# Kernel tuning notes

Measured on AMD Instinct MI355X. Metric: run time of the kernel, lower is better.

Reference implementation:

```python
import jax, jax.numpy as jnp
import numpy as np

B_SZ, T, D_MODEL, N_STATE = 4, 4096, 1024, 256
D_FF = ((int(8 / 3 * D_MODEL) + 7) // 8) * 8  # 2736
EPS = 1e-6


def setup_inputs() -> dict:
    key = jax.random.key(0)
    ks = jax.random.split(key, 8)
    return {
        "x": jax.random.normal(ks[0], (B_SZ, T, D_MODEL), dtype=jnp.float32),
        "log_lambda": jax.random.normal(ks[1], (N_STATE,), dtype=jnp.float32) * 0.5 + 3.0,
        "B_w": jax.random.normal(ks[2], (N_STATE, D_MODEL), dtype=jnp.float32) / np.sqrt(D_MODEL),
        "C_w": jax.random.normal(ks[3], (D_MODEL, N_STATE), dtype=jnp.float32) / np.sqrt(N_STATE),
        "D_skip": jnp.zeros((D_MODEL,), dtype=jnp.float32),
        "ssm_norm_w": jnp.ones((D_MODEL,), dtype=jnp.float32),
        "ffn_norm_w": jnp.ones((D_MODEL,), dtype=jnp.float32),
        "w1": jax.random.normal(ks[4], (D_FF, D_MODEL), dtype=jnp.float32) / np.sqrt(D_MODEL),
        "w2": jax.random.normal(ks[5], (D_MODEL, D_FF), dtype=jnp.float32) / np.sqrt(D_FF),
        "w3": jax.random.normal(ks[6], (D_FF, D_MODEL), dtype=jnp.float32) / np.sqrt(D_MODEL),
    }


def _rmsnorm(x, w):
    rms = jnp.sqrt(jnp.mean(x * x, axis=-1, keepdims=True) + EPS)
    return x / rms * w


def reference(x, log_lambda, B_w, C_w, D_skip, ssm_norm_w, ffn_norm_w, w1, w2, w3):
    # --- SSM branch ---
    u = _rmsnorm(x, ssm_norm_w)                       # [B,T,D]
    lam = jax.nn.sigmoid(log_lambda)                  # [N]
    Bu = jnp.einsum("btd,nd->btn", u, B_w)            # [B,T,N]

    def step(h, bu_t):                                 # h: [B,N], bu_t: [B,N]
        h = lam * h + bu_t
        return h, h

    h0 = jnp.zeros((x.shape[0], log_lambda.shape[0]), dtype=x.dtype)
    _, hs = jax.lax.scan(step, h0, jnp.swapaxes(Bu, 0, 1))  # hs: [T,B,N]
    hs = jnp.swapaxes(hs, 0, 1)                        # [B,T,N]
    y = jnp.einsum("btn,dn->btd", hs, C_w) + D_skip * u
    x = x + y

    # --- FFN branch (SwiGLU) ---
    z = _rmsnorm(x, ffn_norm_w)
    gate = jax.nn.silu(jnp.einsum("btd,fd->btf", z, w1))
    val = jnp.einsum("btd,fd->btf", z, w3)
    ffn = jnp.einsum("btf,df->btd", gate * val, w2)
    return x + ffn
```

## Files before the change

### kernel.cpp

```cpp
#include <hip/hip_runtime.h>
#include <hip/hip_bf16.h>
#include <cstdint>

#define BSZ   4
#define TLEN  4096
#define DM    1024
#define NS    256
#define DFF   2736
#define DFFP  2816
#define NPK   5632
#define NCHUNK 64
#define CLEN   64

typedef __attribute__((ext_vector_type(8))) short bf16x8;
typedef __attribute__((ext_vector_type(4))) float f32x4;

__device__ __forceinline__ float bf2f(ushort u) {
  union { unsigned int i; float f; } v; v.i = ((unsigned int)u) << 16; return v.f;
}
__device__ __forceinline__ ushort f2bf(float f) {
  union { float f; unsigned int i; } v; v.f = f;
  unsigned int r = v.i + 0x7FFFu + ((v.i >> 16) & 1u);
  return (ushort)(r >> 16);
}
__device__ __forceinline__ void gload16(const ushort* g, ushort* l) {
  __builtin_amdgcn_global_load_lds((const __attribute__((address_space(1))) void*)g,
                                   (__attribute__((address_space(3))) void*)l, 16, 0, 0);
}

__global__ void convert_pad(const float* __restrict__ src, ushort* __restrict__ dst,
                            int srcR, int srcC, int dstR, int dstC) {
  long total = (long)dstR * dstC / 4;
  for (long q = (long)blockIdx.x * blockDim.x + threadIdx.x; q < total;
       q += (long)gridDim.x * blockDim.x) {
    long e = q * 4;
    int r = (int)(e / dstC);
    int c = (int)(e % dstC);
    ushort4 o;
    float v0 = (r < srcR && c + 0 < srcC) ? src[(long)r * srcC + c + 0] : 0.f;
    float v1 = (r < srcR && c + 1 < srcC) ? src[(long)r * srcC + c + 1] : 0.f;
    float v2 = (r < srcR && c + 2 < srcC) ? src[(long)r * srcC + c + 2] : 0.f;
    float v3 = (r < srcR && c + 3 < srcC) ? src[(long)r * srcC + c + 3] : 0.f;
    o.x = f2bf(v0); o.y = f2bf(v1); o.z = f2bf(v2); o.w = f2bf(v3);
    *(ushort4*)(dst + e) = o;
  }
}

__global__ void pack_w13(const float* __restrict__ w1, const float* __restrict__ w3,
                         ushort* __restrict__ wp) {
  long total = (long)NPK * DM / 4;
  for (long q = (long)blockIdx.x * blockDim.x + threadIdx.x; q < total;
       q += (long)gridDim.x * blockDim.x) {
    long e = q * 4;
    int r = (int)(e >> 10);
    int c = (int)(e & 1023);
    int f = ((r >> 5) << 4) + (r & 15);
    const float* src = ((r >> 4) & 1) ? w3 : w1;
    ushort4 o;
    if (f < DFF) {
      const float4 v = *(const float4*)(src + (long)f * DM + c);
      o.x = f2bf(v.x); o.y = f2bf(v.y); o.z = f2bf(v.z); o.w = f2bf(v.w);
    } else {
      o.x = o.y = o.z = o.w = 0;
    }
    *(ushort4*)(wp + e) = o;
  }
}

__global__ __launch_bounds__(256) void rmsnorm_bf16(const float* __restrict__ x,
                                                    const float* __restrict__ w,
                                                    ushort* __restrict__ out) {
  long row = blockIdx.x;
  int tid = threadIdx.x;
  const float4* xr = (const float4*)(x + row * DM);
  float4 v = xr[tid];
  float ss = v.x * v.x + v.y * v.y + v.z * v.z + v.w * v.w;
#pragma unroll
  for (int m = 32; m >= 1; m >>= 1) ss += __shfl_xor(ss, m);
  __shared__ float red[4];
  if ((tid & 63) == 0) red[tid >> 6] = ss;
  __syncthreads();
  float tot = red[0] + red[1] + red[2] + red[3];
  float inv = rsqrtf(tot * (1.0f / DM) + 1e-6f);
  float4 wv = ((const float4*)w)[tid];
  ushort4 o;
  o.x = f2bf(v.x * inv * wv.x);
  o.y = f2bf(v.y * inv * wv.y);
  o.z = f2bf(v.z * inv * wv.z);
  o.w = f2bf(v.w * inv * wv.w);
  ((ushort4*)(out + row * DM))[tid] = o;
}

__global__ __launch_bounds__(256) void scan_local(float* __restrict__ Bu,
                                                  float* __restrict__ E,
                                                  const float* __restrict__ loglam) {
  int bc = blockIdx.x;
  int b = bc / NCHUNK, c = bc % NCHUNK;
  int n = threadIdx.x;
  float lam = 1.f / (1.f + __expf(-loglam[n]));
  float h = 0.f;
  long base = ((long)b * TLEN + (long)c * CLEN) * NS + n;
#pragma unroll 4
  for (int t = 0; t < CLEN; ++t) {
    long idx = base + (long)t * NS;
    h = lam * h + Bu[idx];
    Bu[idx] = h;
  }
  E[((long)b * NCHUNK + c) * NS + n] = h;
}

__global__ __launch_bounds__(1024) void scan_carry(const float* __restrict__ E,
                                                   float* __restrict__ C,
                                                   const float* __restrict__ loglam) {
  int tid = threadIdx.x;
  int b = tid >> 8, n = tid & 255;
  float lam = 1.f / (1.f + __expf(-loglam[n]));
  float lamL = lam;
#pragma unroll
  for (int i = 0; i < 6; ++i) lamL *= lamL;
  float carry = 0.f;
  for (int c = 0; c < NCHUNK; ++c) {
    long idx = ((long)b * NCHUNK + c) * NS + n;
    C[idx] = carry;
    carry = lamL * carry + E[idx];
  }
}

__global__ __launch_bounds__(256) void scan_fix(const float* __restrict__ local,
                                                const float* __restrict__ Carry,
                                                const float* __restrict__ loglam,
                                                ushort* __restrict__ hsb) {
  int bc = blockIdx.x;
  int b = bc / NCHUNK, c = bc % NCHUNK;
  int n = threadIdx.x;
  float lam = 1.f / (1.f + __expf(-loglam[n]));
  float p = Carry[((long)b * NCHUNK + c) * NS + n];
  long base = ((long)b * TLEN + (long)c * CLEN) * NS + n;
#pragma unroll 4
  for (int t = 0; t < CLEN; ++t) {
    p *= lam;
    long idx = base + (long)t * NS;
    hsb[idx] = f2bf(local[idx] + p);
  }
}

template <int EPI>
__global__ __launch_bounds__(256, 2) void gemm_bt(
    const ushort* __restrict__ A, const ushort* __restrict__ B0,
    float* __restrict__ outF,
    const float* __restrict__ xin, const float* __restrict__ dskip,
    const ushort* __restrict__ uin, int M, int N, int K) {
  __shared__ ushort sA[128 * 32];
  __shared__ ushort sB[128 * 32];

  int tid = threadIdx.x;
  int lane = tid & 63;
  int wid = tid >> 6;
  int nbx = N >> 7;
  int by = blockIdx.x / nbx;
  int bx = blockIdx.x - by * nbx;
  long brow = (long)by << 7;
  long bcol = (long)bx << 7;

  int srow = tid >> 2;
  int scol = (tid & 3) << 3;
  const ushort* gA = A + (brow + srow) * (long)K + scol;
  const ushort* gB = B0 + (bcol + srow) * (long)K + scol;
  ushort* lA = sA + (wid << 9);
  ushort* lB = sB + (wid << 9);

  int wr = wid >> 1, wc = wid & 1;
  int fr = lane & 15;
  int fk = (lane >> 4) << 3;

  f32x4 acc0[4][4];
#pragma unroll
  for (int i = 0; i < 4; ++i)
#pragma unroll
    for (int j = 0; j < 4; ++j) acc0[i][j] = (f32x4)0.f;

  long rowq = 64 * (long)K;
  for (int kt = 0; kt < K; kt += 32) {
    __syncthreads();
    gload16(gA + kt, lA);
    gload16(gA + kt + rowq, lA + 2048);
    gload16(gB + kt, lB);
    gload16(gB + kt + rowq, lB + 2048);
    __syncthreads();

    bf16x8 a[4], b[4];
#pragma unroll
    for (int i = 0; i < 4; ++i)
      a[i] = *(const bf16x8*)(sA + ((wr * 64 + i * 16 + fr) * 32 + fk));
#pragma unroll
    for (int j = 0; j < 4; ++j)
      b[j] = *(const bf16x8*)(sB + ((wc * 64 + j * 16 + fr) * 32 + fk));
#pragma unroll
    for (int i = 0; i < 4; ++i)
#pragma unroll
      for (int j = 0; j < 4; ++j)
        acc0[i][j] = __builtin_amdgcn_mfma_f32_16x16x32_bf16(a[i], b[j], acc0[i][j], 0, 0, 0);
  }

#pragma unroll
  for (int i = 0; i < 4; ++i) {
    int rowb = wr * 64 + i * 16 + ((lane >> 4) << 2);
#pragma unroll
    for (int j = 0; j < 4; ++j) {
      long gcol = bcol + wc * 64 + j * 16 + fr;
#pragma unroll
      for (int r = 0; r < 4; ++r) {
        long grow = brow + rowb + r;
        long idx = grow * N + gcol;
        float v = acc0[i][j][r];
        if constexpr (EPI == 0) {
          outF[idx] = v;
        } else {
          outF[idx] = v + xin[idx] + dskip[gcol] * bf2f(uin[idx]);
        }
      }
    }
  }
}

template <bool DUAL>
__global__ __launch_bounds__(512, 2) void big_gemm(
    const ushort* __restrict__ A, const ushort* __restrict__ Bm,
    float* __restrict__ outF, ushort* __restrict__ outU) {
  constexpr int K = DUAL ? DM : DFFP;
  constexpr int NT = K / 64;
  constexpr int BUFE = 32768;
  extern __shared__ __align__(16) char smem_raw[];
  ushort* lds = (ushort*)smem_raw;

  int tid = threadIdx.x;
  int lane = tid & 63;
  int wid = tid >> 6;

  int bid = blockIdx.x;
  int chunk = bid & 7;
  int w = bid >> 3;
  int rt = chunk * 8 + (w & 7);
  int ct = w >> 3;
  long brow = (long)rt << 8;
  long bcol = (long)ct << 8;

  uint aOff[4], bOff[4];
  int dstBase[4];
#pragma unroll
  for (int q = 0; q < 4; ++q) {
    int slot = q * 512 + tid;
    int row = slot >> 3, cs = slot & 7;
    int csx = cs ^ (row & 7);
    aOff[q] = (uint)((brow + row) * (long)K + csx * 8);
    bOff[q] = (uint)((bcol + row) * (long)K + csx * 8);
    dstBase[q] = q * 4096 + wid * 512;
  }

  int wm = wid >> 2, wn = wid & 3;
  int fr = lane & 15, fq = lane >> 4;
  int abase = (wm * 128 + fr) * 64;
  int bbase = 16384 + (wn * 64 + fr) * 64;
  int sl0 = ((0 * 4 + fq) ^ (fr & 7)) << 3;
  int sl1 = ((1 * 4 + fq) ^ (fr & 7)) << 3;

  f32x4 acc[8][4];
#pragma unroll
  for (int m = 0; m < 8; ++m)
#pragma unroll
    for (int n = 0; n < 4; ++n) acc[m][n] = (f32x4)0.f;

  auto STAGE = [&](int g, int buf) {
    const ushort* Ag = A + (long)g * 64;
    const ushort* Bg = Bm + (long)g * 64;
    ushort* lb = lds + buf * BUFE;
#pragma unroll
    for (int q = 0; q < 4; ++q) gload16(Ag + aOff[q], lb + dstBase[q]);
#pragma unroll
    for (int q = 0; q < 4; ++q) gload16(Bg + bOff[q], lb + 16384 + dstBase[q]);
  };

  STAGE(0, 0);
#pragma unroll 1
  for (int g = 0; g < NT; ++g) {
    if (g + 1 < NT) {
      STAGE(g + 1, (g + 1) & 1);
      asm volatile("s_waitcnt vmcnt(8)" ::: "memory");
    } else {
      asm volatile("s_waitcnt vmcnt(0)" ::: "memory");
    }
    asm volatile("s_barrier" ::: "memory");
    const ushort* lb = lds + (g & 1) * BUFE;
    {
      bf16x8 a[8], b[4];
#pragma unroll
      for (int m = 0; m < 8; ++m) a[m] = *(const bf16x8*)(lb + abase + m * 1024 + sl0);
#pragma unroll
      for (int n = 0; n < 4; ++n) b[n] = *(const bf16x8*)(lb + bbase + n * 1024 + sl0);
#pragma unroll
      for (int m = 0; m < 8; ++m)
#pragma unroll
        for (int n = 0; n < 4; ++n)
          acc[m][n] = __builtin_amdgcn_mfma_f32_16x16x32_bf16(a[m], b[n], acc[m][n], 0, 0, 0);
    }
    {
      bf16x8 a[8], b[4];
#pragma unroll
      for (int m = 0; m < 8; ++m) a[m] = *(const bf16x8*)(lb + abase + m * 1024 + sl1);
#pragma unroll
      for (int n = 0; n < 4; ++n) b[n] = *(const bf16x8*)(lb + bbase + n * 1024 + sl1);
#pragma unroll
      for (int m = 0; m < 8; ++m)
#pragma unroll
        for (int n = 0; n < 4; ++n)
          acc[m][n] = __builtin_amdgcn_mfma_f32_16x16x32_bf16(a[m], b[n], acc[m][n], 0, 0, 0);
    }
    asm volatile("s_barrier" ::: "memory");
  }

#pragma unroll
  for (int m = 0; m < 8; ++m) {
    int rowb = wm * 128 + m * 16 + fq * 4;
    if constexpr (DUAL) {
#pragma unroll
      for (int jp = 0; jp < 2; ++jp) {
        long fcol = (bcol >> 1) + wn * 32 + jp * 16 + fr;
#pragma unroll
        for (int r = 0; r < 4; ++r) {
          long grow = brow + rowb + r;
          float gt = acc[m][2 * jp][r];
          float vl = acc[m][2 * jp + 1][r];
          float s = gt / (1.f + __expf(-gt));
          outU[grow * DFFP + fcol] = f2bf(s * vl);
        }
      }
    } else {
#pragma unroll
      for (int n = 0; n < 4; ++n) {
        long gcol = bcol + wn * 64 + n * 16 + fr;
#pragma unroll
        for (int r = 0; r < 4; ++r) {
          long grow = brow + rowb + r;
          outF[grow * DM + gcol] += acc[m][n][r];
        }
      }
    }
  }
}

extern "C" void kernel_launch(void* const* d_in, const int* in_sizes, int n_in,
                              void* d_out, int out_size, void* d_ws, size_t ws_size,
                              hipStream_t stream) {
  const float* x      = (const float*)d_in[0];
  const float* loglam = (const float*)d_in[1];
  const float* B_w    = (const float*)d_in[2];
  const float* C_w    = (const float*)d_in[3];
  const float* D_skip = (const float*)d_in[4];
  const float* ssm_w  = (const float*)d_in[5];
  const float* ffn_w  = (const float*)d_in[6];
  const float* w1     = (const float*)d_in[7];
  const float* w2     = (const float*)d_in[8];
  const float* w3     = (const float*)d_in[9];
  float* out = (float*)d_out;

  char* ws = (char*)d_ws;
  ushort* u_bf  = (ushort*)(ws + 0);
  float*  Bu    = (float*) (ws + 33554432);
  ushort* hs_bf = (ushort*)(ws + 50331648);
  float*  E     = (float*) (ws + 58720256);
  float*  Carry = (float*) (ws + 58982400);
  ushort* wB    = (ushort*)(ws + 59244544);
  ushort* wC    = (ushort*)(ws + 59768832);
  ushort* Wp    = (ushort*)(ws + 60293120);
  ushort* w2p   = (ushort*)(ws + 71827456);
  ushort* gv    = (ushort*)(ws + 77594624);

  constexpr int BIG_LDS = 131072;
  (void)hipFuncSetAttribute((const void*)&big_gemm<true>,
                            hipFuncAttributeMaxDynamicSharedMemorySize, BIG_LDS);
  (void)hipFuncSetAttribute((const void*)&big_gemm<false>,
                            hipFuncAttributeMaxDynamicSharedMemorySize, BIG_LDS);

  auto cvb = [](long elems) {
    long q = elems / 4;
    long b = (q + 255) / 256;
    return (int)(b > 4096 ? 4096 : b);
  };

  convert_pad<<<cvb(256L * 1024), 256, 0, stream>>>(B_w, wB, 256, 1024, 256, 1024);
  convert_pad<<<cvb(1024L * 256), 256, 0, stream>>>(C_w, wC, 1024, 256, 1024, 256);
  pack_w13<<<2048, 256, 0, stream>>>(w1, w3, Wp);
  convert_pad<<<cvb(1024L * DFFP), 256, 0, stream>>>(w2, w2p, 1024, DFF, 1024, DFFP);

  rmsnorm_bf16<<<BSZ * TLEN, 256, 0, stream>>>(x, ssm_w, u_bf);
  gemm_bt<0><<<(16384 / 128) * (NS / 128), 256, 0, stream>>>(
      u_bf, wB, Bu, nullptr, nullptr, nullptr, 16384, NS, DM);
  scan_local<<<BSZ * NCHUNK, 256, 0, stream>>>(Bu, E, loglam);
  scan_carry<<<1, 1024, 0, stream>>>(E, Carry, loglam);
  scan_fix<<<BSZ * NCHUNK, 256, 0, stream>>>(Bu, Carry, loglam, hs_bf);
  gemm_bt<1><<<(16384 / 128) * (DM / 128), 256, 0, stream>>>(
      hs_bf, wC, out, x, D_skip, u_bf, 16384, DM, NS);

  rmsnorm_bf16<<<BSZ * TLEN, 256, 0, stream>>>(out, ffn_w, u_bf);
  big_gemm<true><<<8 * 8 * (NPK / 256), 512, BIG_LDS, stream>>>(u_bf, Wp, nullptr, gv);
  big_gemm<false><<<8 * 8 * (DM / 256), 512, BIG_LDS, stream>>>(gv, w2p, out, nullptr);
}
```

Measured before the change: 561.4 us.

## Restructure big GEMM main loop into 8-phase interleaved load/MFMA schedule

```diff
diff --git a/kernel.cpp b/kernel.cpp
--- a/kernel.cpp
+++ b/kernel.cpp
@@ -27,6 +27,7 @@
   __builtin_amdgcn_global_load_lds((const __attribute__((address_space(1))) void*)g,
                                    (__attribute__((address_space(3))) void*)l, 16, 0, 0);
 }
+#define BAR() asm volatile("s_barrier" ::: "memory")
 
 __global__ void convert_pad(const float* __restrict__ src, ushort* __restrict__ dst,
                             int srcR, int srcC, int dstR, int dstC) {
@@ -229,7 +230,7 @@
     float* __restrict__ outF, ushort* __restrict__ outU) {
   constexpr int K = DUAL ? DM : DFFP;
   constexpr int NT = K / 64;
-  constexpr int BUFE = 32768;
+  constexpr int NI = NT / 2;
   extern __shared__ __align__(16) char smem_raw[];
   ushort* lds = (ushort*)smem_raw;
 
@@ -245,24 +246,27 @@
   long brow = (long)rt << 8;
   long bcol = (long)ct << 8;
 
-  uint aOff[4], bOff[4];
-  int dstBase[4];
-#pragma unroll
-  for (int q = 0; q < 4; ++q) {
-    int slot = q * 512 + tid;
-    int row = slot >> 3, cs = slot & 7;
-    int csx = cs ^ (row & 7);
-    aOff[q] = (uint)((brow + row) * (long)K + csx * 8);
-    bOff[q] = (uint)((bcol + row) * (long)K + csx * 8);
-    dstBase[q] = q * 4096 + wid * 512;
+  uint aSrc[2], bSrc[2];
+  int aDst[2], bDst[2];
+#pragma unroll
+  for (int p = 0; p < 2; ++p) {
+    int s = p * 512 + tid;
+    int lr = s >> 3;
+    int cs = s & 7;
+    int csx = cs ^ (lr & 7);
+    int rA = ((lr >> 6) << 7) | (lr & 63);
+    int rB = ((lr >> 5) << 6) | (lr & 31);
+    aSrc[p] = (uint)((brow + rA) * (long)K + csx * 8);
+    bSrc[p] = (uint)((bcol + rB) * (long)K + csx * 8);
+    aDst[p] = (rA & ~7) * 64;
+    bDst[p] = 16384 + (rB & ~7) * 64;
   }
 
   int wm = wid >> 2, wn = wid & 3;
   int fr = lane & 15, fq = lane >> 4;
-  int abase = (wm * 128 + fr) * 64;
-  int bbase = 16384 + (wn * 64 + fr) * 64;
-  int sl0 = ((0 * 4 + fq) ^ (fr & 7)) << 3;
-  int sl1 = ((1 * 4 + fq) ^ (fr & 7)) << 3;
+  int sl[2];
+  sl[0] = ((0 * 4 + fq) ^ (fr & 7)) << 3;
+  sl[1] = ((1 * 4 + fq) ^ (fr & 7)) << 3;
 
   f32x4 acc[8][4];
 #pragma unroll
@@ -270,52 +274,90 @@
 #pragma unroll
     for (int n = 0; n < 4; ++n) acc[m][n] = (f32x4)0.f;
 
-  auto STAGE = [&](int g, int buf) {
-    const ushort* Ag = A + (long)g * 64;
-    const ushort* Bg = Bm + (long)g * 64;
-    ushort* lb = lds + buf * BUFE;
-#pragma unroll
-    for (int q = 0; q < 4; ++q) gload16(Ag + aOff[q], lb + dstBase[q]);
-#pragma unroll
-    for (int q = 0; q < 4; ++q) gload16(Bg + bOff[q], lb + 16384 + dstBase[q]);
-  };
-
-  STAGE(0, 0);
+  bf16x8 afr[4][2];
+  bf16x8 bfr[2][2][2];
+
+  auto STAGE_A = [&](long gk, int d, int half) {
+    const ushort* Ag = A + gk * 64 + (long)half * (64L * K);
+    ushort* lb = lds + d * 32768 + half * 4096;
+#pragma unroll
+    for (int p = 0; p < 2; ++p) gload16(Ag + aSrc[p], lb + aDst[p]);
+  };
+  auto STAGE_B = [&](long gk, int d, int half) {
+    const ushort* Bg = Bm + gk * 64 + (long)half * (32L * K);
+    ushort* lb = lds + d * 32768 + half * 2048;
+#pragma unroll
+    for (int p = 0; p < 2; ++p) gload16(Bg + bSrc[p], lb + bDst[p]);
+  };
+  auto LDA = [&](const ushort* lb, int mh) {
+#pragma unroll
+    for (int i = 0; i < 4; ++i) {
+      int row = wm * 128 + (mh * 4 + i) * 16 + fr;
+#pragma unroll
+      for (int kk = 0; kk < 2; ++kk)
+        afr[i][kk] = *(const bf16x8*)(lb + row * 64 + sl[kk]);
+    }
+  };
+  auto LDB = [&](const ushort* lb, int nh) {
+#pragma unroll
+    for (int j = 0; j < 2; ++j) {
+      int row = wn * 64 + (nh * 2 + j) * 16 + fr;
+#pragma unroll
+      for (int kk = 0; kk < 2; ++kk)
+        bfr[nh][j][kk] = *(const bf16x8*)(lb + 16384 + row * 64 + sl[kk]);
+    }
+  };
+  auto MF = [&](int mh, int nh) {
+    __builtin_amdgcn_s_setprio(1);
+#pragma unroll
+    for (int kk = 0; kk < 2; ++kk)
+#pragma unroll
+      for (int i = 0; i < 4; ++i)
+#pragma unroll
+        for (int j = 0; j < 2; ++j)
+          acc[mh * 4 + i][nh * 2 + j] = __builtin_amdgcn_mfma_f32_16x16x32_bf16(
+              afr[i][kk], bfr[nh][j][kk], acc[mh * 4 + i][nh * 2 + j], 0, 0, 0);
+    __builtin_amdgcn_s_setprio(0);
+  };
+
+  STAGE_A(0, 0, 0); STAGE_B(0, 0, 0); STAGE_B(0, 0, 1); STAGE_A(0, 0, 1);
+  STAGE_A(1, 1, 0); STAGE_B(1, 1, 0); STAGE_B(1, 1, 1);
+  asm volatile("s_waitcnt vmcnt(6)" ::: "memory");
+  BAR();
+
+  const ushort* lb0 = lds;
+  const ushort* lb1 = lds + 32768;
 #pragma unroll 1
-  for (int g = 0; g < NT; ++g) {
-    if (g + 1 < NT) {
-      STAGE(g + 1, (g + 1) & 1);
-      asm volatile("s_waitcnt vmcnt(8)" ::: "memory");
-    } else {
-      asm volatile("s_waitcnt vmcnt(0)" ::: "memory");
-    }
-    asm volatile("s_barrier" ::: "memory");
-    const ushort* lb = lds + (g & 1) * BUFE;
-    {
-      bf16x8 a[8], b[4];
-#pragma unroll
-      for (int m = 0; m < 8; ++m) a[m] = *(const bf16x8*)(lb + abase + m * 1024 + sl0);
-#pragma unroll
-      for (int n = 0; n < 4; ++n) b[n] = *(const bf16x8*)(lb + bbase + n * 1024 + sl0);
-#pragma unroll
-      for (int m = 0; m < 8; ++m)
-#pragma unroll
-        for (int n = 0; n < 4; ++n)
-          acc[m][n] = __builtin_amdgcn_mfma_f32_16x16x32_bf16(a[m], b[n], acc[m][n], 0, 0, 0);
-    }
-    {
-      bf16x8 a[8], b[4];
-#pragma unroll
-      for (int m = 0; m < 8; ++m) a[m] = *(const bf16x8*)(lb + abase + m * 1024 + sl1);
-#pragma unroll
-      for (int n = 0; n < 4; ++n) b[n] = *(const bf16x8*)(lb + bbase + n * 1024 + sl1);
-#pragma unroll
-      for (int m = 0; m < 8; ++m)
-#pragma unroll
-        for (int n = 0; n < 4; ++n)
-          acc[m][n] = __builtin_amdgcn_mfma_f32_16x16x32_bf16(a[m], b[n], acc[m][n], 0, 0, 0);
-    }
-    asm volatile("s_barrier" ::: "memory");
+  for (int u = 0; u < NI; ++u) {
+    long t1 = 2L * u + 1, t2 = 2L * u + 2, t3 = 2L * u + 3;
+    bool nl = (u + 1 < NI);
+    LDA(lb0, 0); LDB(lb0, 0);
+    STAGE_A(t1, 1, 1);
+    BAR(); MF(0, 0); BAR();
+    LDB(lb0, 1);
+    if (nl) STAGE_A(t2, 0, 0);
+    BAR(); MF(0, 1); BAR();
+    LDA(lb0, 1);
+    if (nl) STAGE_B(t2, 0, 0);
+    BAR(); MF(1, 0); BAR();
+    if (nl) STAGE_B(t2, 0, 1);
+    BAR(); MF(1, 1);
+    if (nl) asm volatile("s_waitcnt vmcnt(6)" ::: "memory");
+    else    asm volatile("s_waitcnt vmcnt(0)" ::: "memory");
+    BAR();
+    LDA(lb1, 0); LDB(lb1, 0);
+    if (nl) STAGE_A(t2, 0, 1);
+    BAR(); MF(0, 0); BAR();
+    LDB(lb1, 1);
+    if (nl) STAGE_A(t3, 1, 0);
+    BAR(); MF(0, 1); BAR();
+    LDA(lb1, 1);
+    if (nl) STAGE_B(t3, 1, 0);
+    BAR(); MF(1, 0); BAR();
+    if (nl) STAGE_B(t3, 1, 1);
+    BAR(); MF(1, 1);
+    if (nl) asm volatile("s_waitcnt vmcnt(6)" ::: "memory");
+    BAR();
   }
 
 #pragma unroll
```

Result: slower. 594.2 us (+5.8%).
